# Kernel tuning notes

Hardware: AMD Instinct MI355X
Metric: run time of the kernel (lower is better)

The kernel has to match this reference:

```python
import jax, jax.numpy as jnp
import numpy as np

A, G, P, C = 250000, 64, 4096, 2
LOW, HIGH = 0.3, 0.7
BETA = 1.0 / 9.0
IMG = 800.0


def _make_boxes(key, n):
    k1, k2 = jax.random.split(key)
    xy = jax.random.uniform(k1, (n, 2), minval=0.0, maxval=IMG - 130.0)
    wh = jax.random.uniform(k2, (n, 2), minval=8.0, maxval=128.0)
    return jnp.concatenate([xy, xy + wh], axis=1)


def setup_inputs():
    ks = jax.random.split(jax.random.key(0), 11)
    return {
        "anchors": _make_boxes(ks[0], A),
        "gt_boxes": _make_boxes(ks[1], G),
        "gt_score_labels": jax.random.uniform(ks[2], (G,)),
        "gt_confidence_labels": jax.random.randint(ks[3], (G,), 0, 2),
        "objectness": jax.random.normal(ks[4], (A,)),
        "pred_bbox_deltas": jax.random.normal(ks[5], (A, 4)) * 0.1,
        "class_logits": jax.random.normal(ks[6], (P, C)),
        "box_regression": jax.random.normal(ks[7], (P, C * 4)) * 0.1,
        "roi_labels": jax.random.randint(ks[8], (P,), 0, C),
        "roi_regression_targets": jax.random.normal(ks[9], (P, 4)) * 0.1,
        "roi_scores": jax.random.uniform(ks[10], (P,)),
    }


def box_iou(a, b):
    # a: [G,4], b: [A,4] -> [G,A]
    area_a = (a[:, 2] - a[:, 0]) * (a[:, 3] - a[:, 1])
    area_b = (b[:, 2] - b[:, 0]) * (b[:, 3] - b[:, 1])
    lt = jnp.maximum(a[:, None, :2], b[None, :, :2])
    rb = jnp.minimum(a[:, None, 2:], b[None, :, 2:])
    wh = jnp.clip(rb - lt, 0.0)
    inter = wh[..., 0] * wh[..., 1]
    return inter / (area_a[:, None] + area_b[None, :] - inter)


def encode_boxes(gt, anchors):
    # torchvision BoxCoder.encode with unit weights
    aw = anchors[:, 2] - anchors[:, 0]
    ah = anchors[:, 3] - anchors[:, 1]
    acx = anchors[:, 0] + 0.5 * aw
    acy = anchors[:, 1] + 0.5 * ah
    gw = gt[:, 2] - gt[:, 0]
    gh = gt[:, 3] - gt[:, 1]
    gcx = gt[:, 0] + 0.5 * gw
    gcy = gt[:, 1] + 0.5 * gh
    return jnp.stack([(gcx - acx) / aw, (gcy - acy) / ah,
                      jnp.log(gw / aw), jnp.log(gh / ah)], axis=1)


def smooth_l1(d):
    ad = jnp.abs(d)
    return jnp.where(ad < BETA, 0.5 * d * d / BETA, ad - 0.5 * BETA)


def reference(anchors, gt_boxes, gt_score_labels, gt_confidence_labels, objectness,
              pred_bbox_deltas, class_logits, box_regression, roi_labels,
              roi_regression_targets, roi_scores):
    # ---- assign_targets_to_anchors (Matcher with low-quality matches) ----
    iou = box_iou(gt_boxes, anchors)            # [G, A]
    matched_vals = iou.max(axis=0)              # [A]
    all_matches = iou.argmax(axis=0)            # [A]
    matched_idxs = jnp.where(matched_vals < LOW, -1,
                   jnp.where(matched_vals < HIGH, -2, all_matches))
    best_per_gt = iou.max(axis=1, keepdims=True)            # [G,1]
    force = (iou == best_per_gt).any(axis=0)                # [A]
    matched_idxs = jnp.where(force, all_matches, matched_idxs)
    clamped = jnp.clip(matched_idxs, 0)
    matched_gt = gt_boxes[clamped]                          # [A,4]
    labels = (matched_idxs >= 0).astype(jnp.float32)
    labels = jnp.minimum(labels, gt_score_labels[clamped])
    labels = jnp.where(matched_idxs == -1, 0.0, labels)     # BELOW_LOW_THRESHOLD
    labels = jnp.where(matched_idxs == -2, -1.0, labels)    # BETWEEN_THRESHOLDS
    labels = jnp.where((gt_confidence_labels[clamped] == 0) & (matched_idxs >= 0), -1.0, labels)
    reg_targets = encode_boxes(matched_gt, anchors)         # [A,4]

    # ---- my_rpn_compute_loss (deterministic full pos/neg selection) ----
    pos = labels >= 1.0
    neg = labels == 0.0
    n_samp = pos.astype(jnp.float32).sum() + neg.astype(jnp.float32).sum()
    sl = smooth_l1(pred_bbox_deltas - reg_targets).sum(axis=-1)
    rpn_box_loss = (sl * pos).sum() / n_samp
    sel = pos | neg
    y = jnp.where(sel, jnp.clip(labels, 0.0, 1.0), 0.0)
    x = objectness
    bce = jnp.maximum(x, 0.0) - x * y + jnp.log1p(jnp.exp(-jnp.abs(x)))
    objectness_loss = (bce * sel).sum() / n_samp

    # ---- my_roi_loss ----
    fixed_labels = jnp.stack([1.0 - roi_scores, roi_scores], axis=1)  # [P,2]
    log_probs = jax.nn.log_softmax(class_logits, axis=1)
    classification_loss = jnp.mean(-(fixed_labels * log_probs).sum(axis=1))
    br = box_regression.reshape(P, C, 4)
    idx = jnp.broadcast_to(jnp.clip(roi_labels, 0)[:, None, None], (P, 1, 4))
    br_sel = jnp.take_along_axis(br, idx, axis=1)[:, 0]               # [P,4]
    pos_roi = (roi_labels > 0).astype(jnp.float32)
    roi_box_loss = (smooth_l1(br_sel - roi_regression_targets).sum(axis=-1) * pos_roi).sum() / P

    return jnp.stack([objectness_loss, rpn_box_loss, classification_loss, roi_box_loss])
```

## Files before the change

kernel.cpp:

```cpp
#include <hip/hip_runtime.h>
#include <hip/hip_bf16.h>
#include <math.h>

#define NA 250000
#define NG 64
#define NP 4096

#define SPAN 512
#define NB ((NA + SPAN - 1) / SPAN)
#define NBP 512
#define RBLK (NP / 256)

#define OFF_TAB    0
#define OFF_MAXARG (OFF_TAB + NG * NBP)
#define OFF_ROI    (OFF_MAXARG + 2 * NB * SPAN)
#define OFF_SUM    (OFF_ROI + RBLK * 2)
#define OFF_CNT    (OFF_SUM + NB * 4)


static __device__ __forceinline__ float area_of(float4 b) {
#pragma clang fp contract(off)
    return (b.z - b.x) * (b.w - b.y);
}

static __device__ __forceinline__ float iou_one(
    float gx0, float gy0, float gx1, float gy1, float ga,
    float ax0, float ay0, float ax1, float ay1, float aa)
{
#pragma clang fp contract(off)
    float ltx = fmaxf(gx0, ax0);
    float lty = fmaxf(gy0, ay0);
    float rbx = fminf(gx1, ax1);
    float rby = fminf(gy1, ay1);
    float w = fmaxf(rbx - ltx, 0.0f);
    float h = fmaxf(rby - lty, 0.0f);
    float inter = w * h;
    float uni = ga + aa - inter;
    return inter * __builtin_amdgcn_rcpf(uni);
}

static __device__ __forceinline__ float smooth_l1_f(float d) {
    const float BETA = 1.0f / 9.0f;
    float ad = fabsf(d);
    return (ad < BETA) ? (0.5f * d * d / BETA) : (ad - 0.5f * BETA);
}


__global__ __launch_bounds__(256) void kA(const float4* __restrict__ anchors,
                                          const float4* __restrict__ gt,
                                          const float* __restrict__ logits,
                                          const float* __restrict__ breg,
                                          const int* __restrict__ rlab,
                                          const float4* __restrict__ rtgt,
                                          const float* __restrict__ rsc,
                                          float* __restrict__ ws) {
    int t = threadIdx.x;
    int b = blockIdx.x;

    if (b >= NB) {
        int r = b - NB;
        if (r == 0 && t == 0) *(int*)(ws + OFF_CNT) = 0;
        if (t < NBP - NB) {
#pragma unroll
            for (int row = 0; row < 4; row++)
                ws[OFF_TAB + (4 * r + row) * NBP + NB + t] = 0.0f;
        }
        __shared__ float rbuf[4][2];
        int p = r * 256 + t;
        float l0 = logits[2 * p], l1 = logits[2 * p + 1];
        float mx = fmaxf(l0, l1);
        float lse = mx + __logf(__expf(l0 - mx) + __expf(l1 - mx));
        float s = rsc[p];
        float clsl = -((1.0f - s) * (l0 - lse) + s * (l1 - lse));

        int lbl = rlab[p];
        int cl = lbl < 0 ? 0 : lbl;
        float4 bb = *(const float4*)(breg + 8 * p + 4 * cl);
        float4 tg = rtgt[p];
        float sl = smooth_l1_f(bb.x - tg.x) + smooth_l1_f(bb.y - tg.y) +
                   smooth_l1_f(bb.z - tg.z) + smooth_l1_f(bb.w - tg.w);
        float boxl = (lbl > 0) ? sl : 0.0f;

        int lane = t & 63, w = t >> 6;
        for (int off = 32; off > 0; off >>= 1) {
            clsl += __shfl_down(clsl, off);
            boxl += __shfl_down(boxl, off);
        }
        if (lane == 0) { rbuf[w][0] = clsl; rbuf[w][1] = boxl; }
        __syncthreads();
        if (t == 0) {
            float s0 = 0.f, s1 = 0.f;
            for (int i = 0; i < 4; i++) { s0 += rbuf[i][0]; s1 += rbuf[i][1]; }
            ws[OFF_ROI + 2 * r] = s0;
            ws[OFF_ROI + 2 * r + 1] = s1;
        }
        return;
    }

    int a0 = b * SPAN + t;
    int a1 = a0 + 256;
    bool ok0 = a0 < NA, ok1 = a1 < NA;
    float4 av0 = ok0 ? anchors[a0] : make_float4(0.f, 0.f, 0.f, 0.f);
    float4 av1 = ok1 ? anchors[a1] : make_float4(0.f, 0.f, 0.f, 0.f);
    float aa0 = area_of(av0);
    float aa1 = area_of(av1);

    float m[NG];
#pragma unroll
    for (int g = 0; g < NG; g++) m[g] = 0.0f;

    float max0 = -1.0f, max1 = -1.0f;
    int arg0 = 0, arg1 = 0;
#pragma unroll
    for (int g = 0; g < NG; g++) {
        float4 G = gt[g];
        float ga = area_of(G);
        float u0 = iou_one(G.x, G.y, G.z, G.w, ga, av0.x, av0.y, av0.z, av0.w, aa0);
        float u1 = iou_one(G.x, G.y, G.z, G.w, ga, av1.x, av1.y, av1.z, av1.w, aa1);
        if (u0 > max0) { max0 = u0; arg0 = g; }
        if (u1 > max1) { max1 = u1; arg1 = g; }
        m[g] = fmaxf(m[g], fmaxf(u0, u1));
    }

    float2* ma = (float2*)(ws + OFF_MAXARG);
    if (ok0) ma[a0] = make_float2(max0, __int_as_float(arg0));
    if (ok1) ma[a1] = make_float2(max1, __int_as_float(arg1));

    __shared__ float sred[4][NG];
    int lane = t & 63, w = t >> 6;
#pragma unroll
    for (int g = 0; g < NG; g++) {
        float mm = m[g];
        for (int off = 32; off > 0; off >>= 1)
            mm = fmaxf(mm, __shfl_down(mm, off));
        if (lane == 0) sred[w][g] = mm;
    }
    __syncthreads();
    if (t < NG) {
        float mm = fmaxf(fmaxf(sred[0][t], sred[1][t]),
                         fmaxf(sred[2][t], sred[3][t]));
        ws[OFF_TAB + t * NBP + b] = mm;
    }
}


__global__ __launch_bounds__(256) void kB(const float4* __restrict__ anchors,
                                          const float* __restrict__ objness,
                                          const float4* __restrict__ pdel,
                                          const float4* __restrict__ gt,
                                          const float* __restrict__ gscore,
                                          const int* __restrict__ gconf,
                                          float* __restrict__ ws,
                                          float* __restrict__ out) {
    __shared__ float sbest[NG];
    __shared__ int   scand[NG];
    __shared__ int   scnt;
    __shared__ float rbuf[4][4];
    __shared__ bool  islast;

    int t = threadIdx.x;
    int b = blockIdx.x;
    int lane = t & 63, w = t >> 6;

    if (t == 0) scnt = 0;

    {
        int g = t >> 2, quad = t & 3;
        const float4* rowv = (const float4*)(ws + OFF_TAB + g * NBP + quad * 128);
        float mm = 0.0f;
#pragma unroll
        for (int j = 0; j < 32; j++) {
            float4 v = rowv[j];
            mm = fmaxf(mm, fmaxf(fmaxf(v.x, v.y), fmaxf(v.z, v.w)));
        }
        mm = fmaxf(mm, __shfl_xor(mm, 1));
        mm = fmaxf(mm, __shfl_xor(mm, 2));
        if (quad == 0) sbest[g] = mm;
    }
    __syncthreads();

    if (t < NG) {
        if (ws[OFF_TAB + t * NBP + b] == sbest[t]) {
            int i = atomicAdd(&scnt, 1);
            scand[i] = t;
        }
    }
    __syncthreads();
    int cnt = scnt;

    const float2* ma = (const float2*)(ws + OFF_MAXARG);

    float posf = 0.f, negf = 0.f, slpos = 0.f, bces = 0.f;
#pragma unroll
    for (int k = 0; k < 2; k++) {
        int a = b * SPAN + k * 256 + t;
        if (a >= NA) continue;
        float2 mv = ma[a];
        float maxv = mv.x;
        int arg = __float_as_int(mv.y);

        float4 av = anchors[a];
        float aa = area_of(av);

        bool force = false;
        for (int i = 0; i < cnt; i++) {
            int g = scand[i];
            float4 G = gt[g];
            float ga = area_of(G);
            float u = iou_one(G.x, G.y, G.z, G.w, ga, av.x, av.y, av.z, av.w, aa);
            force |= (u == sbest[g]);
        }

        int matched = (maxv < 0.3f) ? -1 : ((maxv < 0.7f) ? -2 : arg);
        if (force) matched = arg;
        int cl = matched < 0 ? 0 : matched;

        float4 Ac = gt[cl];
        float score = gscore[cl];
        int conf = gconf[cl];
        float label = (matched >= 0) ? 1.0f : 0.0f;
        label = fminf(label, score);
        if (matched == -1) label = 0.0f;
        if (matched == -2) label = -1.0f;
        if (conf == 0 && matched >= 0) label = -1.0f;

        bool pos = (label >= 1.0f);
        bool neg = (label == 0.0f);
        bool sel = pos || neg;

        float aw = av.z - av.x, ah = av.w - av.y;
        float acx = av.x + 0.5f * aw, acy = av.y + 0.5f * ah;
        float gw = Ac.z - Ac.x, gh = Ac.w - Ac.y;
        float gcx = Ac.x + 0.5f * gw, gcy = Ac.y + 0.5f * gh;
        float t0 = (gcx - acx) / aw;
        float t1 = (gcy - acy) / ah;
        float t2 = __logf(gw / aw);
        float t3 = __logf(gh / ah);

        float4 pd = pdel[a];
        float sl = smooth_l1_f(pd.x - t0) + smooth_l1_f(pd.y - t1) +
                   smooth_l1_f(pd.z - t2) + smooth_l1_f(pd.w - t3);

        float x = objness[a];
        float y = sel ? fminf(fmaxf(label, 0.0f), 1.0f) : 0.0f;
        float bce = fmaxf(x, 0.0f) - x * y + __logf(1.0f + __expf(-fabsf(x)));

        if (pos) { posf += 1.0f; slpos += sl; }
        if (neg) negf += 1.0f;
        if (sel) bces += bce;
    }

    for (int off = 32; off > 0; off >>= 1) {
        posf  += __shfl_down(posf, off);
        negf  += __shfl_down(negf, off);
        slpos += __shfl_down(slpos, off);
        bces  += __shfl_down(bces, off);
    }
    if (lane == 0) { rbuf[w][0] = posf; rbuf[w][1] = negf; rbuf[w][2] = slpos; rbuf[w][3] = bces; }
    __syncthreads();
    if (t == 0) {
        float s0 = 0.f, s1 = 0.f, s2 = 0.f, s3 = 0.f;
        for (int i = 0; i < 4; i++) { s0 += rbuf[i][0]; s1 += rbuf[i][1]; s2 += rbuf[i][2]; s3 += rbuf[i][3]; }
        float* r = ws + OFF_SUM + 4 * b;
        r[0] = s0; r[1] = s1; r[2] = s2; r[3] = s3;
        __threadfence();
        int prev = atomicAdd((int*)(ws + OFF_CNT), 1);
        islast = (prev == NB - 1);
    }
    __syncthreads();
    if (!islast) return;
    __threadfence();

    __shared__ double sredc[4][6];
    double a0 = 0, a1 = 0, a2 = 0, a3 = 0, c0 = 0, c1 = 0;
    for (int r = t; r < NB; r += 256) {
        const float4 v = *(const float4*)(ws + OFF_SUM + 4 * r);
        a0 += v.x; a1 += v.y; a2 += v.z; a3 += v.w;
    }
    if (t < RBLK) {
        c0 = ws[OFF_ROI + 2 * t];
        c1 = ws[OFF_ROI + 2 * t + 1];
    }
    for (int off = 32; off > 0; off >>= 1) {
        a0 += __shfl_down(a0, off);
        a1 += __shfl_down(a1, off);
        a2 += __shfl_down(a2, off);
        a3 += __shfl_down(a3, off);
        c0 += __shfl_down(c0, off);
        c1 += __shfl_down(c1, off);
    }
    if (lane == 0) {
        sredc[w][0] = a0; sredc[w][1] = a1; sredc[w][2] = a2;
        sredc[w][3] = a3; sredc[w][4] = c0; sredc[w][5] = c1;
    }
    __syncthreads();
    if (t == 0) {
        double s[6] = {0, 0, 0, 0, 0, 0};
        for (int i = 0; i < 4; i++)
            for (int j = 0; j < 6; j++) s[j] += sredc[i][j];
        double n = s[0] + s[1];
        out[0] = (float)(s[3] / n);
        out[1] = (float)(s[2] / n);
        out[2] = (float)(s[4] / (double)NP);
        out[3] = (float)(s[5] / (double)NP);
    }
}

extern "C" void kernel_launch(void* const* d_in, const int* in_sizes, int n_in,
                              void* d_out, int out_size, void* d_ws, size_t ws_size,
                              hipStream_t stream) {
    const float4* anchors = (const float4*)d_in[0];
    const float4* gt      = (const float4*)d_in[1];
    const float*  gscore  = (const float*)d_in[2];
    const int*    gconf   = (const int*)d_in[3];
    const float*  objness = (const float*)d_in[4];
    const float4* pdel    = (const float4*)d_in[5];
    const float*  clog    = (const float*)d_in[6];
    const float*  breg    = (const float*)d_in[7];
    const int*    rlab    = (const int*)d_in[8];
    const float4* rtgt    = (const float4*)d_in[9];
    const float*  rsc     = (const float*)d_in[10];

    float* ws = (float*)d_ws;
    float* out = (float*)d_out;

    kA<<<NB + RBLK, 256, 0, stream>>>(anchors, gt, clog, breg, rlab, rtgt, rsc, ws);
    kB<<<NB, 256, 0, stream>>>(anchors, objness, pdel, gt, gscore, gconf, ws, out);
}
```

Before: 123.0 us.

## Fold per-anchor loss into IoU kernel and patch forced matches in single-block finalizer

```diff
diff --git a/kernel.cpp b/kernel.cpp
--- a/kernel.cpp
+++ b/kernel.cpp
@@ -1,5 +1,4 @@
 #include <hip/hip_runtime.h>
-#include <hip/hip_bf16.h>
 #include <math.h>
 
 #define NA 250000
@@ -15,7 +14,9 @@
 #define OFF_MAXARG (OFF_TAB + NG * NBP)
 #define OFF_ROI    (OFF_MAXARG + 2 * NB * SPAN)
 #define OFF_SUM    (OFF_ROI + RBLK * 2)
-#define OFF_CNT    (OFF_SUM + NB * 4)
+
+#define CAND_MAX 256
+#define FMAX 512
 
 
 static __device__ __forceinline__ float area_of(float4 b) {
@@ -45,6 +46,48 @@
     return (ad < BETA) ? (0.5f * d * d / BETA) : (ad - 0.5f * BETA);
 }
 
+static __device__ __forceinline__ void contrib_noforce(
+    float4 av, float maxv, int arg, float4 pd, float x,
+    const float4* __restrict__ gt, const float* __restrict__ gscore,
+    const int* __restrict__ gconf,
+    float& posf, float& negf, float& slpos, float& bces)
+{
+    int matched = (maxv < 0.3f) ? -1 : ((maxv < 0.7f) ? -2 : arg);
+    int cl = matched < 0 ? 0 : matched;
+
+    float4 Ac = gt[cl];
+    float score = gscore[cl];
+    int conf = gconf[cl];
+    float label = (matched >= 0) ? 1.0f : 0.0f;
+    label = fminf(label, score);
+    if (matched == -1) label = 0.0f;
+    if (matched == -2) label = -1.0f;
+    if (conf == 0 && matched >= 0) label = -1.0f;
+
+    bool pos = (label >= 1.0f);
+    bool neg = (label == 0.0f);
+    bool sel = pos || neg;
+
+    float aw = av.z - av.x, ah = av.w - av.y;
+    float acx = av.x + 0.5f * aw, acy = av.y + 0.5f * ah;
+    float gw = Ac.z - Ac.x, gh = Ac.w - Ac.y;
+    float gcx = Ac.x + 0.5f * gw, gcy = Ac.y + 0.5f * gh;
+    float t0 = (gcx - acx) / aw;
+    float t1 = (gcy - acy) / ah;
+    float t2 = __logf(gw / aw);
+    float t3 = __logf(gh / ah);
+
+    float sl = smooth_l1_f(pd.x - t0) + smooth_l1_f(pd.y - t1) +
+               smooth_l1_f(pd.z - t2) + smooth_l1_f(pd.w - t3);
+
+    float y = sel ? fminf(fmaxf(label, 0.0f), 1.0f) : 0.0f;
+    float bce = fmaxf(x, 0.0f) - x * y + __logf(1.0f + __expf(-fabsf(x)));
+
+    if (pos) { posf += 1.0f; slpos += sl; }
+    if (neg) negf += 1.0f;
+    if (sel) bces += bce;
+}
+
 
 __global__ __launch_bounds__(256) void kA(const float4* __restrict__ anchors,
                                           const float4* __restrict__ gt,
@@ -53,19 +96,22 @@
                                           const int* __restrict__ rlab,
                                           const float4* __restrict__ rtgt,
                                           const float* __restrict__ rsc,
+                                          const float* __restrict__ objness,
+                                          const float4* __restrict__ pdel,
+                                          const float* __restrict__ gscore,
+                                          const int* __restrict__ gconf,
                                           float* __restrict__ ws) {
     int t = threadIdx.x;
     int b = blockIdx.x;
 
     if (b >= NB) {
         int r = b - NB;
-        if (r == 0 && t == 0) *(int*)(ws + OFF_CNT) = 0;
         if (t < NBP - NB) {
 #pragma unroll
             for (int row = 0; row < 4; row++)
                 ws[OFF_TAB + (4 * r + row) * NBP + NB + t] = 0.0f;
         }
-        __shared__ float rbuf[4][2];
+        __shared__ float rbuf2[4][2];
         int p = r * 256 + t;
         float l0 = logits[2 * p], l1 = logits[2 * p + 1];
         float mx = fmaxf(l0, l1);
@@ -86,11 +132,11 @@
             clsl += __shfl_down(clsl, off);
             boxl += __shfl_down(boxl, off);
         }
-        if (lane == 0) { rbuf[w][0] = clsl; rbuf[w][1] = boxl; }
+        if (lane == 0) { rbuf2[w][0] = clsl; rbuf2[w][1] = boxl; }
         __syncthreads();
         if (t == 0) {
             float s0 = 0.f, s1 = 0.f;
-            for (int i = 0; i < 4; i++) { s0 += rbuf[i][0]; s1 += rbuf[i][1]; }
+            for (int i = 0; i < 4; i++) { s0 += rbuf2[i][0]; s1 += rbuf2[i][1]; }
             ws[OFF_ROI + 2 * r] = s0;
             ws[OFF_ROI + 2 * r + 1] = s1;
         }
@@ -106,9 +152,6 @@
     float aa1 = area_of(av1);
 
     float m[NG];
-#pragma unroll
-    for (int g = 0; g < NG; g++) m[g] = 0.0f;
-
     float max0 = -1.0f, max1 = -1.0f;
     int arg0 = 0, arg1 = 0;
 #pragma unroll
@@ -119,135 +162,50 @@
         float u1 = iou_one(G.x, G.y, G.z, G.w, ga, av1.x, av1.y, av1.z, av1.w, aa1);
         if (u0 > max0) { max0 = u0; arg0 = g; }
         if (u1 > max1) { max1 = u1; arg1 = g; }
-        m[g] = fmaxf(m[g], fmaxf(u0, u1));
+        m[g] = fmaxf(u0, u1);
     }
 
     float2* ma = (float2*)(ws + OFF_MAXARG);
     if (ok0) ma[a0] = make_float2(max0, __int_as_float(arg0));
     if (ok1) ma[a1] = make_float2(max1, __int_as_float(arg1));
 
+    int lane = t & 63, w = t >> 6;
+
+#pragma unroll
+    for (int s = 0; s < 6; s++) {
+        int half = 32 >> s;
+        bool up = (lane >> s) & 1;
+#pragma unroll
+        for (int j = 0; j < half; j++) {
+            float mine = up ? m[j] : m[j + half];
+            float keep = up ? m[j + half] : m[j];
+            float oth  = __shfl_xor(mine, 1 << s);
+            m[j] = fmaxf(keep, oth);
+        }
+    }
+    int grev = ((lane & 1) << 5) | ((lane & 2) << 3) | ((lane & 4) << 1) |
+               ((lane & 8) >> 1) | ((lane & 16) >> 3) | ((lane & 32) >> 5);
     __shared__ float sred[4][NG];
-    int lane = t & 63, w = t >> 6;
-#pragma unroll
-    for (int g = 0; g < NG; g++) {
-        float mm = m[g];
-        for (int off = 32; off > 0; off >>= 1)
-            mm = fmaxf(mm, __shfl_down(mm, off));
-        if (lane == 0) sred[w][g] = mm;
-    }
+    sred[w][grev] = m[0];
     __syncthreads();
     if (t < NG) {
         float mm = fmaxf(fmaxf(sred[0][t], sred[1][t]),
                          fmaxf(sred[2][t], sred[3][t]));
         ws[OFF_TAB + t * NBP + b] = mm;
     }
-}
-
-
-__global__ __launch_bounds__(256) void kB(const float4* __restrict__ anchors,
-                                          const float* __restrict__ objness,
-                                          const float4* __restrict__ pdel,
-                                          const float4* __restrict__ gt,
-                                          const float* __restrict__ gscore,
-                                          const int* __restrict__ gconf,
-                                          float* __restrict__ ws,
-                                          float* __restrict__ out) {
-    __shared__ float sbest[NG];
-    __shared__ int   scand[NG];
-    __shared__ int   scnt;
-    __shared__ float rbuf[4][4];
-    __shared__ bool  islast;
-
-    int t = threadIdx.x;
-    int b = blockIdx.x;
-    int lane = t & 63, w = t >> 6;
-
-    if (t == 0) scnt = 0;
-
-    {
-        int g = t >> 2, quad = t & 3;
-        const float4* rowv = (const float4*)(ws + OFF_TAB + g * NBP + quad * 128);
-        float mm = 0.0f;
-#pragma unroll
-        for (int j = 0; j < 32; j++) {
-            float4 v = rowv[j];
-            mm = fmaxf(mm, fmaxf(fmaxf(v.x, v.y), fmaxf(v.z, v.w)));
-        }
-        mm = fmaxf(mm, __shfl_xor(mm, 1));
-        mm = fmaxf(mm, __shfl_xor(mm, 2));
-        if (quad == 0) sbest[g] = mm;
-    }
-    __syncthreads();
-
-    if (t < NG) {
-        if (ws[OFF_TAB + t * NBP + b] == sbest[t]) {
-            int i = atomicAdd(&scnt, 1);
-            scand[i] = t;
-        }
-    }
-    __syncthreads();
-    int cnt = scnt;
-
-    const float2* ma = (const float2*)(ws + OFF_MAXARG);
 
     float posf = 0.f, negf = 0.f, slpos = 0.f, bces = 0.f;
-#pragma unroll
-    for (int k = 0; k < 2; k++) {
-        int a = b * SPAN + k * 256 + t;
-        if (a >= NA) continue;
-        float2 mv = ma[a];
-        float maxv = mv.x;
-        int arg = __float_as_int(mv.y);
-
-        float4 av = anchors[a];
-        float aa = area_of(av);
-
-        bool force = false;
-        for (int i = 0; i < cnt; i++) {
-            int g = scand[i];
-            float4 G = gt[g];
-            float ga = area_of(G);
-            float u = iou_one(G.x, G.y, G.z, G.w, ga, av.x, av.y, av.z, av.w, aa);
-            force |= (u == sbest[g]);
-        }
-
-        int matched = (maxv < 0.3f) ? -1 : ((maxv < 0.7f) ? -2 : arg);
-        if (force) matched = arg;
-        int cl = matched < 0 ? 0 : matched;
-
-        float4 Ac = gt[cl];
-        float score = gscore[cl];
-        int conf = gconf[cl];
-        float label = (matched >= 0) ? 1.0f : 0.0f;
-        label = fminf(label, score);
-        if (matched == -1) label = 0.0f;
-        if (matched == -2) label = -1.0f;
-        if (conf == 0 && matched >= 0) label = -1.0f;
-
-        bool pos = (label >= 1.0f);
-        bool neg = (label == 0.0f);
-        bool sel = pos || neg;
-
-        float aw = av.z - av.x, ah = av.w - av.y;
-        float acx = av.x + 0.5f * aw, acy = av.y + 0.5f * ah;
-        float gw = Ac.z - Ac.x, gh = Ac.w - Ac.y;
-        float gcx = Ac.x + 0.5f * gw, gcy = Ac.y + 0.5f * gh;
-        float t0 = (gcx - acx) / aw;
-        float t1 = (gcy - acy) / ah;
-        float t2 = __logf(gw / aw);
-        float t3 = __logf(gh / ah);
-
-        float4 pd = pdel[a];
-        float sl = smooth_l1_f(pd.x - t0) + smooth_l1_f(pd.y - t1) +
-                   smooth_l1_f(pd.z - t2) + smooth_l1_f(pd.w - t3);
-
-        float x = objness[a];
-        float y = sel ? fminf(fmaxf(label, 0.0f), 1.0f) : 0.0f;
-        float bce = fmaxf(x, 0.0f) - x * y + __logf(1.0f + __expf(-fabsf(x)));
-
-        if (pos) { posf += 1.0f; slpos += sl; }
-        if (neg) negf += 1.0f;
-        if (sel) bces += bce;
+    if (ok0) {
+        float4 pd = pdel[a0];
+        float x = objness[a0];
+        contrib_noforce(av0, max0, arg0, pd, x, gt, gscore, gconf,
+                        posf, negf, slpos, bces);
+    }
+    if (ok1) {
+        float4 pd = pdel[a1];
+        float x = objness[a1];
+        contrib_noforce(av1, max1, arg1, pd, x, gt, gscore, gconf,
+                        posf, negf, slpos, bces);
     }
 
     for (int off = 32; off > 0; off >>= 1) {
@@ -256,6 +214,7 @@
         slpos += __shfl_down(slpos, off);
         bces  += __shfl_down(bces, off);
     }
+    __shared__ float rbuf[4][4];
     if (lane == 0) { rbuf[w][0] = posf; rbuf[w][1] = negf; rbuf[w][2] = slpos; rbuf[w][3] = bces; }
     __syncthreads();
     if (t == 0) {
@@ -263,44 +222,157 @@
         for (int i = 0; i < 4; i++) { s0 += rbuf[i][0]; s1 += rbuf[i][1]; s2 += rbuf[i][2]; s3 += rbuf[i][3]; }
         float* r = ws + OFF_SUM + 4 * b;
         r[0] = s0; r[1] = s1; r[2] = s2; r[3] = s3;
-        __threadfence();
-        int prev = atomicAdd((int*)(ws + OFF_CNT), 1);
-        islast = (prev == NB - 1);
-    }
-    __syncthreads();
-    if (!islast) return;
-    __threadfence();
-
+    }
+}
+
+
+__global__ __launch_bounds__(1024) void kFC(const float4* __restrict__ anchors,
+                                            const float4* __restrict__ gt,
+                                            const float* __restrict__ objness,
+                                            const float4* __restrict__ pdel,
+                                            const float* __restrict__ gscore,
+                                            const int* __restrict__ gconf,
+                                            float* __restrict__ ws,
+                                            float* __restrict__ out) {
+    __shared__ float sbest[NG];
+    __shared__ int   cand[CAND_MAX];
+    __shared__ int   ccnt, fcnt;
+    __shared__ int   flist[FMAX];
+    __shared__ float sdn[FMAX], sdb[FMAX], sds[FMAX];
     __shared__ double sredc[4][6];
+
+    int t = threadIdx.x;
+    int lane = t & 63, w = t >> 6;
+    if (t == 0) { ccnt = 0; fcnt = 0; }
+    __syncthreads();
+
+#pragma unroll
+    for (int i = 0; i < 4; i++) {
+        int g = w * 4 + i;
+        const float* row = ws + OFF_TAB + g * NBP;
+        float v[8];
+        float mm = 0.0f;
+#pragma unroll
+        for (int p = 0; p < 8; p++) v[p] = row[lane + 64 * p];
+#pragma unroll
+        for (int p = 0; p < 8; p++) mm = fmaxf(mm, v[p]);
+#pragma unroll
+        for (int off = 1; off < 64; off <<= 1)
+            mm = fmaxf(mm, __shfl_xor(mm, off));
+        if (lane == 0) sbest[g] = mm;
+#pragma unroll
+        for (int p = 0; p < 8; p++) {
+            if (v[p] == mm) {
+                int idx = atomicAdd(&ccnt, 1);
+                if (idx < CAND_MAX) cand[idx] = (g << 16) | (lane + 64 * p);
+            }
+        }
+    }
+    __syncthreads();
+
+    const float2* ma = (const float2*)(ws + OFF_MAXARG);
+    int nc = min(ccnt, CAND_MAX);
+    int tot = nc << 9;
+    for (int idx = t; idx < tot; idx += 1024) {
+        int e = idx >> 9, i = idx & 511;
+        int gs = cand[e];
+        int g = gs >> 16, s = gs & 0xffff;
+        int a = s * SPAN + i;
+        if (a >= NA) continue;
+        float bestg = sbest[g];
+        float2 mv = ma[a];
+        if (mv.x < bestg || mv.x >= 0.7f) continue;
+        float4 G = gt[g];
+        float4 av = anchors[a];
+        float u = iou_one(G.x, G.y, G.z, G.w, area_of(G),
+                          av.x, av.y, av.z, av.w, area_of(av));
+        if (u == bestg) {
+            int fi = atomicAdd(&fcnt, 1);
+            if (fi < FMAX) flist[fi] = a;
+        }
+    }
+    __syncthreads();
+
+    int fc = min(fcnt, FMAX);
+    for (int i = t; i < fc; i += 1024) {
+        int a = flist[i];
+        bool dup = false;
+        for (int j = 0; j < i; j++) dup = dup || (flist[j] == a);
+        float dN = 0.f, dB = 0.f, dS = 0.f;
+        if (!dup) {
+            float2 mv = ma[a];
+            float maxv = mv.x;
+            int arg = __float_as_int(mv.y);
+            float x = objness[a];
+            float bceY0 = fmaxf(x, 0.0f) + __logf(1.0f + __expf(-fabsf(x)));
+            float n0 = 0.f, b0 = 0.f;
+            if (maxv < 0.3f) { n0 = 1.0f; b0 = bceY0; }
+            float sc = gscore[arg];
+            int cf = gconf[arg];
+            float label1 = fminf(1.0f, sc);
+            if (cf == 0) label1 = -1.0f;
+            bool pos1 = (label1 >= 1.0f);
+            bool neg1 = (label1 == 0.0f);
+            bool sel1 = pos1 || neg1;
+            float n1 = (pos1 ? 1.f : 0.f) + (neg1 ? 1.f : 0.f);
+            float y1 = sel1 ? fminf(fmaxf(label1, 0.0f), 1.0f) : 0.0f;
+            float b1 = sel1 ? (fmaxf(x, 0.0f) - x * y1 +
+                               __logf(1.0f + __expf(-fabsf(x)))) : 0.0f;
+            float s1v = 0.f;
+            if (pos1) {
+                float4 av = anchors[a];
+                float4 Ac = gt[arg];
+                float4 pd = pdel[a];
+                float aw = av.z - av.x, ah = av.w - av.y;
+                float acx = av.x + 0.5f * aw, acy = av.y + 0.5f * ah;
+                float gw = Ac.z - Ac.x, gh = Ac.w - Ac.y;
+                float gcx = Ac.x + 0.5f * gw, gcy = Ac.y + 0.5f * gh;
+                float t0v = (gcx - acx) / aw, t1v = (gcy - acy) / ah;
+                float t2v = __logf(gw / aw), t3v = __logf(gh / ah);
+                s1v = smooth_l1_f(pd.x - t0v) + smooth_l1_f(pd.y - t1v) +
+                      smooth_l1_f(pd.z - t2v) + smooth_l1_f(pd.w - t3v);
+            }
+            dN = n1 - n0;
+            dB = b1 - b0;
+            dS = s1v;
+        }
+        sdn[i] = dN; sdb[i] = dB; sds[i] = dS;
+    }
+    __syncthreads();
+
     double a0 = 0, a1 = 0, a2 = 0, a3 = 0, c0 = 0, c1 = 0;
-    for (int r = t; r < NB; r += 256) {
-        const float4 v = *(const float4*)(ws + OFF_SUM + 4 * r);
-        a0 += v.x; a1 += v.y; a2 += v.z; a3 += v.w;
-    }
-    if (t < RBLK) {
-        c0 = ws[OFF_ROI + 2 * t];
-        c1 = ws[OFF_ROI + 2 * t + 1];
-    }
-    for (int off = 32; off > 0; off >>= 1) {
-        a0 += __shfl_down(a0, off);
-        a1 += __shfl_down(a1, off);
-        a2 += __shfl_down(a2, off);
-        a3 += __shfl_down(a3, off);
-        c0 += __shfl_down(c0, off);
-        c1 += __shfl_down(c1, off);
-    }
-    if (lane == 0) {
-        sredc[w][0] = a0; sredc[w][1] = a1; sredc[w][2] = a2;
-        sredc[w][3] = a3; sredc[w][4] = c0; sredc[w][5] = c1;
+    if (t < 256) {
+        for (int r = t; r < NB; r += 256) {
+            const float4 v = *(const float4*)(ws + OFF_SUM + 4 * r);
+            a0 += v.x; a1 += v.y; a2 += v.z; a3 += v.w;
+        }
+        if (t < RBLK) {
+            c0 = ws[OFF_ROI + 2 * t];
+            c1 = ws[OFF_ROI + 2 * t + 1];
+        }
+        for (int off = 32; off > 0; off >>= 1) {
+            a0 += __shfl_down(a0, off);
+            a1 += __shfl_down(a1, off);
+            a2 += __shfl_down(a2, off);
+            a3 += __shfl_down(a3, off);
+            c0 += __shfl_down(c0, off);
+            c1 += __shfl_down(c1, off);
+        }
+        if (lane == 0) {
+            sredc[w][0] = a0; sredc[w][1] = a1; sredc[w][2] = a2;
+            sredc[w][3] = a3; sredc[w][4] = c0; sredc[w][5] = c1;
+        }
     }
     __syncthreads();
     if (t == 0) {
         double s[6] = {0, 0, 0, 0, 0, 0};
         for (int i = 0; i < 4; i++)
             for (int j = 0; j < 6; j++) s[j] += sredc[i][j];
-        double n = s[0] + s[1];
-        out[0] = (float)(s[3] / n);
-        out[1] = (float)(s[2] / n);
+        double Dn = 0, Db = 0, Ds = 0;
+        for (int i = 0; i < fc; i++) { Dn += sdn[i]; Db += sdb[i]; Ds += sds[i]; }
+        double n = s[0] + s[1] + Dn;
+        out[0] = (float)((s[3] + Db) / n);
+        out[1] = (float)((s[2] + Ds) / n);
         out[2] = (float)(s[4] / (double)NP);
         out[3] = (float)(s[5] / (double)NP);
     }
@@ -324,6 +396,7 @@
     float* ws = (float*)d_ws;
     float* out = (float*)d_out;
 
-    kA<<<NB + RBLK, 256, 0, stream>>>(anchors, gt, clog, breg, rlab, rtgt, rsc, ws);
-    kB<<<NB, 256, 0, stream>>>(anchors, objness, pdel, gt, gscore, gconf, ws, out);
-}
+    kA<<<NB + RBLK, 256, 0, stream>>>(anchors, gt, clog, breg, rlab, rtgt, rsc,
+                                      objness, pdel, gscore, gconf, ws);
+    kFC<<<1, 1024, 0, stream>>>(anchors, gt, objness, pdel, gscore, gconf, ws, out);
+}
```

Result: faster. 113.0 us (-8.1%).
